# Kernel optimization log

Hardware: AMD Instinct MI355X
Metric: run time of the kernel (lower is better)

## Reference

```python
import jax, jax.numpy as jnp
import numpy as np

NUM_CLASSES = 2
LOG2_NC = float(np.log2(NUM_CLASSES))


def _conv(x, w, b=None):
    # NCHW conv, stride 1, SAME padding (kernel 3 pad 1 or kernel 1 pad 0)
    y = jax.lax.conv_general_dilated(x, w, (1, 1), 'SAME',
                                     dimension_numbers=('NCHW', 'OIHW', 'NCHW'))
    if b is not None:
        y = y + b[None, :, None, None]
    return y


def _uncertainty_map(ds):
    # entropy over class dim, thresholded to {0,1}
    logp = jax.nn.log_softmax(ds, axis=1)            # [B,C,H,W]
    prob = jnp.exp(logp)
    # torch uses log2(prob + 1e-6); replicate exactly
    ent = -jnp.sum(prob * jnp.log2(prob + 1e-6), axis=1) / LOG2_NC  # [B,H,W]
    return (ent >= 0.001).astype(jnp.float32)


def _unob(tar, amap):
    # vectorized UnoB with S=3: interior pixels with tar!=0 get pro=0 unless
    # 4*tar == sum of the 4-neighborhood (i.e. locally constant label)
    t = tar  # [B,H,W] int
    nb = t[:, 2:, 1:-1] + t[:, :-2, 1:-1] + t[:, 1:-1, 2:] + t[:, 1:-1, :-2]
    center = t[:, 1:-1, 1:-1]
    inner_pro = jnp.where((center != 0) & (4 * center != nb), 0.0, 1.0)
    pro = jnp.ones_like(amap)
    pro = pro.at[:, 1:-1, 1:-1].set(inner_pro)
    return amap * pro


def setup_inputs() -> dict:
    key = jax.random.key(0)
    ks = jax.random.split(key, 6)
    B, C, H, W = 8, 128, 128, 128
    return {
        'x': jax.random.normal(ks[0], (B, C, H, W), jnp.float32),
        'skip': jax.random.normal(ks[1], (B, C, H, W), jnp.float32),
        'tar': jax.random.randint(ks[2], (B, 1, H, W), 0, NUM_CLASSES, jnp.int64)
            if jax.config.jax_enable_x64 else
            jax.random.randint(ks[2], (B, 1, H, W), 0, NUM_CLASSES).astype(jnp.int32),
        'W1': jax.random.normal(ks[3], (128, 256, 3, 3), jnp.float32) * 0.05,
        'b1': jnp.zeros((128,), jnp.float32),
        'W2': jax.random.normal(ks[4], (128, 128, 3, 3), jnp.float32) * 0.05,
        'b2': jnp.zeros((128,), jnp.float32),
        'Wds': jax.random.normal(ks[5], (NUM_CLASSES, 128, 1, 1), jnp.float32) * 0.05,
    }


def reference(x, skip, tar, W1, b1, W2, b2, Wds):
    h = jnp.concatenate([x, skip], axis=1)            # [B,2*dim,H,W]
    h = jax.nn.leaky_relu(_conv(h, W1, b1), 0.01)     # [B,dim,H,W]
    h = jax.nn.leaky_relu(_conv(h, W2, b2), 0.01)
    ds = _conv(h, Wds)                                # [B,num_classes,H,W]
    amap = _uncertainty_map(ds)                       # [B,H,W]
    amap = _unob(tar[:, 0], amap)                     # UnoB refinement, S=3
    return h, ds, amap
```

## Files before the change

kernel.cpp:

```cpp
#include <hip/hip_runtime.h>

typedef float f32x16 __attribute__((ext_vector_type(16)));
typedef short bf16x8 __attribute__((ext_vector_type(8)));
typedef unsigned int u32;

static __device__ __forceinline__ unsigned short f2bf(float f) {
  union { float f; unsigned int u; } v;
  v.f = f;
  return (unsigned short)((v.u + 0x7FFFu + ((v.u >> 16) & 1u)) >> 16);
}

static __device__ __forceinline__ void gl_lds16(const unsigned short* g,
                                                unsigned short* l) {
  __builtin_amdgcn_global_load_lds(
      (const __attribute__((address_space(1))) u32*)g,
      (__attribute__((address_space(3))) u32*)l, 16, 0, 0);
}

#define VMCNT4 asm volatile("s_waitcnt vmcnt(4)" ::: "memory")
#define VMCNT0 asm volatile("s_waitcnt vmcnt(0)" ::: "memory")
#define LGKM0 asm volatile("s_waitcnt lgkmcnt(0)" ::: "memory")
#define BAR __builtin_amdgcn_s_barrier()
#define SCHEDB __builtin_amdgcn_sched_barrier(0)

__global__ __launch_bounds__(256) void convert_weights(
    const float* __restrict__ W1, const float* __restrict__ W2,
    unsigned short* __restrict__ W1b, unsigned short* __restrict__ W2b,
    unsigned short* __restrict__ zp) {
  if (blockIdx.x == 1728) {
    uint4* z = (uint4*)zp;
    z[threadIdx.x] = make_uint4(0, 0, 0, 0);
    z[256 + threadIdx.x] = make_uint4(0, 0, 0, 0);
    return;
  }
  int i = blockIdx.x * 256 + threadIdx.x;
  if (i < 294912) {
    int e = i & 7, co = (i >> 3) & 127, r = i >> 10;
    int tap = r % 9, pc = r / 9;
    int ci = (pc >> 1) * 16 + (pc & 1) * 8 + e;
    W1b[i] = f2bf(W1[(co * 256 + ci) * 9 + tap]);
  } else {
    int j = i - 294912;
    if (j < 147456) {
      int e = j & 7, co = (j >> 3) & 127, r = j >> 10;
      int tap = r % 9, pc = r / 9;
      int ci = (pc >> 1) * 16 + (pc & 1) * 8 + e;
      W2b[j] = f2bf(W2[(co * 128 + ci) * 9 + tap]);
    }
  }
}

__global__ __launch_bounds__(256) void transpose_to_bf16(
    const float* __restrict__ src, unsigned short* __restrict__ dst, int cigb) {
  int row = blockIdx.x;
  int b = row >> 7, y = row & 127;
  const float* s = src + (long)b * 128 * 16384 + (long)y * 128;
  for (int it = 0; it < 8; ++it) {
    int u = it * 256 + (int)threadIdx.x;
    int cig = u >> 7, px = u & 127;
    unsigned short pk[8];
#pragma unroll
    for (int e = 0; e < 8; ++e)
      pk[e] = f2bf(s[(long)(cig * 8 + e) * 16384 + px]);
    uint4 vv;
    vv.x = (unsigned)pk[0] | ((unsigned)pk[1] << 16);
    vv.y = (unsigned)pk[2] | ((unsigned)pk[3] << 16);
    vv.z = (unsigned)pk[4] | ((unsigned)pk[5] << 16);
    vv.w = (unsigned)pk[6] | ((unsigned)pk[7] << 16);
    *(uint4*)(&dst[(((long)row * 32 + cigb + cig) * 130 + px + 1) * 8]) = vv;
  }
  if (cigb == 0 && threadIdx.x < 64) {
    int g = threadIdx.x >> 1;
    long col = (threadIdx.x & 1) * 129L;
    *(uint4*)(&dst[(((long)row * 32 + g) * 130 + col) * 8]) = make_uint4(0, 0, 0, 0);
  }
}

template <int CIN, bool FUSE_DS>
__global__ __launch_bounds__(256, 2) void conv3x3(
    const unsigned short* __restrict__ src,
    const unsigned short* __restrict__ wt,
    const float* __restrict__ bias,
    const unsigned short* __restrict__ zp,
    unsigned short* __restrict__ dst_bf16,
    float* __restrict__ dst_f32,
    const float* __restrict__ wds,
    const int* __restrict__ tar,
    float* __restrict__ ds,
    float* __restrict__ amap) {
  constexpr int CPG = CIN / 8;
  constexpr int NC = CIN / 16;
  __shared__ unsigned short in_tile[2][1040 * 8];
  __shared__ unsigned short wt_tile[2304 * 8];
  __shared__ float sb[128];
  __shared__ float w0s[128], w1s[128];
  __shared__ float sc[2 * 4 * 2 * 32];

  const int tid = threadIdx.x;
  const int b = blockIdx.x >> 6;
  const int y0 = (blockIdx.x & 63) * 2;
  const int lane = tid & 63, wave = tid >> 6;
  const int wco = wave & 1, wrow = wave >> 1;
  const int l31 = lane & 31, kh = lane >> 5;

  if (tid < 128) {
    sb[tid] = bias[tid];
    if constexpr (FUSE_DS) {
      w0s[tid] = wds[tid];
      w1s[tid] = wds[128 + tid];
    }
  }

#define STAGE_IN(cic, bufi)                                                    \
  {                                                                            \
    _Pragma("unroll") for (int j = 0; j < 4; ++j) {                            \
      int o = wave * 4 + j;                                                    \
      int s = o * 64 + lane;                                                   \
      int p = s >= 520;                                                        \
      int r = s - p * 520;                                                     \
      int hy = r / 130;                                                        \
      int hx = r - hy * 130;                                                   \
      int gy = y0 - 1 + hy;                                                    \
      const unsigned short* g =                                                \
          (gy >= 0 && gy < 128)                                                \
              ? src + ((size_t)((b * 128 + gy) * CPG) + (size_t)(cic)*2 + p) * \
                          1040 +                                               \
                    hx * 8                                                     \
              : zp + lane * 8;                                                 \
      gl_lds16(g, &in_tile[bufi][(size_t)o * 512]);                            \
    }                                                                          \
  }

#define STAGE_WT(cic)                                                          \
  {                                                                            \
    const unsigned short* wslab = wt + (size_t)(cic)*18432;                    \
    _Pragma("unroll") for (int j = 0; j < 9; ++j) {                            \
      int o = wave * 9 + j;                                                    \
      gl_lds16(wslab + o * 512 + lane * 8, &wt_tile[(size_t)o * 512]);         \
    }                                                                          \
  }

#define LOAD_TAIL(cic, v)                                                      \
  {                                                                            \
    if (tid < 16) {                                                            \
      int gy_ = y0 + 2;                                                        \
      if (gy_ < 128)                                                           \
        v = *(const uint4*)(src +                                              \
                            ((size_t)((b * 128 + gy_) * CPG) +                 \
                             (size_t)(cic)*2 + 1) *                            \
                                1040 +                                         \
                            (114 + tid) * 8);                                  \
    }                                                                          \
  }

#define WRITE_TAIL(bufi, v)                                                    \
  {                                                                            \
    if (tid < 16) *(uint4*)(&in_tile[bufi][(size_t)(1024 + tid) * 8]) = v;     \
  }

  f32x16 acc[2][4] = {};

  {
    uint4 tv = make_uint4(0, 0, 0, 0);
    LOAD_TAIL(0, tv);
    STAGE_IN(0, 0);
    VMCNT0;
    WRITE_TAIL(0, tv);
    LGKM0;
    BAR;
    SCHEDB;
  }

  for (int cic = 0; cic < NC; ++cic) {
    const int cur = cic & 1;
    const bool more = (cic + 1 < NC);
    uint4 tl = make_uint4(0, 0, 0, 0);
    if (more) LOAD_TAIL(cic + 1, tl);
    STAGE_WT(cic);
    if (more) {
      STAGE_IN(cic + 1, cur ^ 1);
      VMCNT4;
      SCHEDB;
      WRITE_TAIL(cur ^ 1, tl);
    } else {
      VMCNT0;
      SCHEDB;
    }
    LGKM0;
    BAR;
    SCHEDB;

    const unsigned short* it = in_tile[cur];
    const size_t wb = (size_t)kh * 9216;
    const size_t ib = (size_t)kh * 4160;
#pragma unroll
    for (int ky = 0; ky < 3; ++ky) {
      const int hy = ky + wrow;
#pragma unroll
      for (int kx = 0; kx < 3; ++kx) {
        const int t = ky * 3 + kx;
        bf16x8 a0 = *(const bf16x8*)(&wt_tile[wb + (size_t)(t * 128 + wco * 64 + l31) * 8]);
        bf16x8 a1 = *(const bf16x8*)(&wt_tile[wb + (size_t)(t * 128 + wco * 64 + 32 + l31) * 8]);
        bf16x8 b0 = *(const bf16x8*)(&it[ib + (size_t)(hy * 130 + l31 + kx) * 8]);
        bf16x8 b1 = *(const bf16x8*)(&it[ib + (size_t)(hy * 130 + 32 + l31 + kx) * 8]);
        bf16x8 b2 = *(const bf16x8*)(&it[ib + (size_t)(hy * 130 + 64 + l31 + kx) * 8]);
        bf16x8 b3 = *(const bf16x8*)(&it[ib + (size_t)(hy * 130 + 96 + l31 + kx) * 8]);
        acc[0][0] = __builtin_amdgcn_mfma_f32_32x32x16_bf16(a0, b0, acc[0][0], 0, 0, 0);
        acc[0][1] = __builtin_amdgcn_mfma_f32_32x32x16_bf16(a0, b1, acc[0][1], 0, 0, 0);
        acc[0][2] = __builtin_amdgcn_mfma_f32_32x32x16_bf16(a0, b2, acc[0][2], 0, 0, 0);
        acc[0][3] = __builtin_amdgcn_mfma_f32_32x32x16_bf16(a0, b3, acc[0][3], 0, 0, 0);
        acc[1][0] = __builtin_amdgcn_mfma_f32_32x32x16_bf16(a1, b0, acc[1][0], 0, 0, 0);
        acc[1][1] = __builtin_amdgcn_mfma_f32_32x32x16_bf16(a1, b1, acc[1][1], 0, 0, 0);
        acc[1][2] = __builtin_amdgcn_mfma_f32_32x32x16_bf16(a1, b2, acc[1][2], 0, 0, 0);
        acc[1][3] = __builtin_amdgcn_mfma_f32_32x32x16_bf16(a1, b3, acc[1][3], 0, 0, 0);
      }
    }
    SCHEDB;
    LGKM0;
    BAR;
    SCHEDB;
  }

  const int gyo = y0 + wrow;
  float pd[4][2] = {};
#pragma unroll
  for (int fc = 0; fc < 2; ++fc) {
#pragma unroll
    for (int fp = 0; fp < 4; ++fp) {
      const int px = fp * 32 + l31;
      if constexpr (!FUSE_DS) {
#pragma unroll
        for (int rg = 0; rg < 4; ++rg) {
          const int co0 = wco * 64 + fc * 32 + rg * 8 + kh * 4;
          unsigned short pk[4];
#pragma unroll
          for (int q = 0; q < 4; ++q) {
            float v = acc[fc][fp][rg * 4 + q] + sb[co0 + q];
            v = v > 0.f ? v : 0.01f * v;
            pk[q] = f2bf(v);
          }
          uint2 o;
          o.x = (unsigned)pk[0] | ((unsigned)pk[1] << 16);
          o.y = (unsigned)pk[2] | ((unsigned)pk[3] << 16);
          *(uint2*)(&dst_bf16[(((long)(b * 128 + gyo) * 16 + (co0 >> 3)) * 130 + px + 1) * 8 +
                              kh * 4]) = o;
        }
      } else {
#pragma unroll
        for (int rg = 0; rg < 4; ++rg) {
          const int co0 = wco * 64 + fc * 32 + rg * 8 + kh * 4;
          float4 wv0 = *(const float4*)(&w0s[co0]);
          float4 wv1 = *(const float4*)(&w1s[co0]);
#pragma unroll
          for (int q = 0; q < 4; ++q) {
            float v = acc[fc][fp][rg * 4 + q] + sb[co0 + q];
            v = v > 0.f ? v : 0.01f * v;
            dst_f32[((long)(b * 128 + co0 + q) << 14) + (gyo << 7) + px] = v;
            float wq0 = (q == 0) ? wv0.x : (q == 1) ? wv0.y : (q == 2) ? wv0.z : wv0.w;
            float wq1 = (q == 0) ? wv1.x : (q == 1) ? wv1.y : (q == 2) ? wv1.z : wv1.w;
            pd[fp][0] += wq0 * v;
            pd[fp][1] += wq1 * v;
          }
        }
      }
    }
  }

  if constexpr (!FUSE_DS) {
    if (tid < 64) {
      int row = tid >> 5, g = (tid >> 1) & 15;
      long col = (tid & 1) * 129L;
      *(uint4*)(&dst_bf16[(((long)(b * 128 + y0 + row) * 16 + g) * 130 + col) * 8]) =
          make_uint4(0, 0, 0, 0);
    }
  } else {
#pragma unroll
    for (int fp = 0; fp < 4; ++fp)
#pragma unroll
      for (int c = 0; c < 2; ++c)
        pd[fp][c] += __shfl_xor(pd[fp][c], 32, 64);
    if (wco == 1 && kh == 0) {
#pragma unroll
      for (int fp = 0; fp < 4; ++fp)
#pragma unroll
        for (int c = 0; c < 2; ++c)
          sc[((wrow * 4 + fp) * 2 + c) * 32 + l31] = pd[fp][c];
    }
    __syncthreads();
    if (wco == 0 && kh == 0) {
      const int* tb = tar + (long)b * 16384;
#pragma unroll
      for (int fp = 0; fp < 4; ++fp) {
        const int px = fp * 32 + l31;
        float a0 = pd[fp][0] + sc[((wrow * 4 + fp) * 2 + 0) * 32 + l31];
        float a1 = pd[fp][1] + sc[((wrow * 4 + fp) * 2 + 1) * 32 + l31];
        ds[((long)b * 2) * 16384 + (gyo << 7) + px] = a0;
        ds[((long)b * 2 + 1) * 16384 + (gyo << 7) + px] = a1;
        float m = fmaxf(a0, a1);
        float e0 = expf(a0 - m), e1 = expf(a1 - m);
        float s = e0 + e1;
        float p0f = e0 / s, p1f = e1 / s;
        float ent = -(p0f * log2f(p0f + 1e-6f) + p1f * log2f(p1f + 1e-6f));
        float un = ent >= 0.001f ? 1.f : 0.f;
        float pro = 1.f;
        if (gyo > 0 && gyo < 127 && px > 0 && px < 127) {
          int c = tb[(gyo << 7) + px];
          if (c != 0) {
            int nb2 = tb[((gyo - 1) << 7) + px] + tb[((gyo + 1) << 7) + px] +
                      tb[(gyo << 7) + px - 1] + tb[(gyo << 7) + px + 1];
            if (4 * c != nb2) pro = 0.f;
          }
        }
        amap[((long)(b * 128 + gyo) << 7) + px] = un * pro;
      }
    }
  }
#undef STAGE_IN
#undef STAGE_WT
#undef LOAD_TAIL
#undef WRITE_TAIL
}

extern "C" void kernel_launch(void* const* d_in, const int* in_sizes, int n_in,
                              void* d_out, int out_size, void* d_ws, size_t ws_size,
                              hipStream_t stream) {
  const float* x    = (const float*)d_in[0];
  const float* skip = (const float*)d_in[1];
  const int*   tar  = (const int*)d_in[2];
  const float* W1   = (const float*)d_in[3];
  const float* b1   = (const float*)d_in[4];
  const float* W2   = (const float*)d_in[5];
  const float* b2   = (const float*)d_in[6];
  const float* Wds  = (const float*)d_in[7];

  float* out_h  = (float*)d_out;
  float* out_ds = out_h + 16777216;
  float* out_am = out_ds + 262144;

  unsigned short* W1b = (unsigned short*)d_ws;
  unsigned short* W2b = W1b + 294912;
  unsigned short* zp  = W2b + 147456;
  unsigned short* h1  = (unsigned short*)((char*)d_ws + (1u << 20));

  unsigned short* h0 = (unsigned short*)d_out;

  convert_weights<<<1729, 256, 0, stream>>>(W1, W2, W1b, W2b, zp);
  transpose_to_bf16<<<1024, 256, 0, stream>>>(x, h0, 0);
  transpose_to_bf16<<<1024, 256, 0, stream>>>(skip, h0, 16);
  conv3x3<256, false><<<512, 256, 0, stream>>>(h0, W1b, b1, zp, h1, nullptr,
                                               nullptr, nullptr, nullptr, nullptr);
  conv3x3<128, true><<<512, 256, 0, stream>>>(h1, W2b, b2, zp, nullptr, out_h,
                                              Wds, tar, out_ds, out_am);
}
```

Before: 154.9 us.

## Double conv tile to 4 rows with 512 threads and double-buffer weight staging

Each conv block now covers 4 output rows with 8 waves instead of 2 rows with 4 waves, so each staged weight slab is reused across twice as many output pixels and the grid drops to 256 blocks. Weights are now double-buffered alongside the input tile, and all async global-to-LDS copies are precomputed into per-thread base pointers and strides, issued 8 per thread each iteration. The separate tail-load path for the halo is removed. The cost is more LDS per block, which can limit occupancy, and only 256 blocks to spread over the GPU's compute units.

```diff
diff --git a/kernel.cpp b/kernel.cpp
--- a/kernel.cpp
+++ b/kernel.cpp
@@ -17,7 +17,7 @@
       (__attribute__((address_space(3))) u32*)l, 16, 0, 0);
 }
 
-#define VMCNT4 asm volatile("s_waitcnt vmcnt(4)" ::: "memory")
+#define VMCNT8 asm volatile("s_waitcnt vmcnt(8)" ::: "memory")
 #define VMCNT0 asm volatile("s_waitcnt vmcnt(0)" ::: "memory")
 #define LGKM0 asm volatile("s_waitcnt lgkmcnt(0)" ::: "memory")
 #define BAR __builtin_amdgcn_s_barrier()
@@ -77,7 +77,7 @@
 }
 
 template <int CIN, bool FUSE_DS>
-__global__ __launch_bounds__(256, 2) void conv3x3(
+__global__ __launch_bounds__(512, 2) void conv3x3(
     const unsigned short* __restrict__ src,
     const unsigned short* __restrict__ wt,
     const float* __restrict__ bias,
@@ -90,15 +90,16 @@
     float* __restrict__ amap) {
   constexpr int CPG = CIN / 8;
   constexpr int NC = CIN / 16;
-  __shared__ unsigned short in_tile[2][1040 * 8];
-  __shared__ unsigned short wt_tile[2304 * 8];
+  __shared__ unsigned short in_tile[2][1664 * 8];
+  __shared__ unsigned short wt_tile[2][2304 * 8];
+  __shared__ unsigned short scr[64 * 8];
   __shared__ float sb[128];
   __shared__ float w0s[128], w1s[128];
-  __shared__ float sc[2 * 4 * 2 * 32];
+  __shared__ float sc[4 * 4 * 2 * 32];
 
   const int tid = threadIdx.x;
-  const int b = blockIdx.x >> 6;
-  const int y0 = (blockIdx.x & 63) * 2;
+  const int b = blockIdx.x >> 5;
+  const int y0 = (blockIdx.x & 31) * 4;
   const int lane = tid & 63, wave = tid >> 6;
   const int wco = wave & 1, wrow = wave >> 1;
   const int l31 = lane & 31, kh = lane >> 5;
@@ -111,96 +112,77 @@
     }
   }
 
-#define STAGE_IN(cic, bufi)                                                    \
-  {                                                                            \
-    _Pragma("unroll") for (int j = 0; j < 4; ++j) {                            \
-      int o = wave * 4 + j;                                                    \
-      int s = o * 64 + lane;                                                   \
-      int p = s >= 520;                                                        \
-      int r = s - p * 520;                                                     \
-      int hy = r / 130;                                                        \
-      int hx = r - hy * 130;                                                   \
-      int gy = y0 - 1 + hy;                                                    \
-      const unsigned short* g =                                                \
-          (gy >= 0 && gy < 128)                                                \
-              ? src + ((size_t)((b * 128 + gy) * CPG) + (size_t)(cic)*2 + p) * \
-                          1040 +                                               \
-                    hx * 8                                                     \
-              : zp + lane * 8;                                                 \
-      gl_lds16(g, &in_tile[bufi][(size_t)o * 512]);                            \
-    }                                                                          \
-  }
-
-#define STAGE_WT(cic)                                                          \
-  {                                                                            \
-    const unsigned short* wslab = wt + (size_t)(cic)*18432;                    \
-    _Pragma("unroll") for (int j = 0; j < 9; ++j) {                            \
-      int o = wave * 9 + j;                                                    \
-      gl_lds16(wslab + o * 512 + lane * 8, &wt_tile[(size_t)o * 512]);         \
-    }                                                                          \
-  }
-
-#define LOAD_TAIL(cic, v)                                                      \
-  {                                                                            \
-    if (tid < 16) {                                                            \
-      int gy_ = y0 + 2;                                                        \
-      if (gy_ < 128)                                                           \
-        v = *(const uint4*)(src +                                              \
-                            ((size_t)((b * 128 + gy_) * CPG) +                 \
-                             (size_t)(cic)*2 + 1) *                            \
-                                1040 +                                         \
-                            (114 + tid) * 8);                                  \
-    }                                                                          \
-  }
-
-#define WRITE_TAIL(bufi, v)                                                    \
-  {                                                                            \
-    if (tid < 16) *(uint4*)(&in_tile[bufi][(size_t)(1024 + tid) * 8]) = v;     \
+  const unsigned short* gb[8];
+  unsigned short* ld0[8];
+  int gst[8];
+  int lst[8];
+#pragma unroll
+  for (int i = 0; i < 8; ++i) {
+    const int o = wave * 8 + i;
+    if (o < 36) {
+      gb[i] = wt + o * 512 + lane * 8;
+      gst[i] = 18432;
+      ld0[i] = &wt_tile[0][(size_t)o * 512];
+      lst[i] = 18432;
+    } else if (o < 62) {
+      const int q = o - 36;
+      const int p = q / 13, j = q - p * 13;
+      const int s = j * 64 + lane;
+      const int hy = s / 130, hx = s - hy * 130;
+      const int gy = y0 - 1 + hy;
+      const bool ok = (s < 780) && (gy >= 0) && (gy < 128);
+      gb[i] = ok ? src + ((size_t)((b * 128 + gy) * CPG) + p) * 1040 + hx * 8
+                 : zp + lane * 8;
+      gst[i] = ok ? 2080 : 0;
+      ld0[i] = &in_tile[0][(size_t)(p * 832 + j * 64) * 8];
+      lst[i] = 1664 * 8;
+    } else {
+      gb[i] = zp + lane * 8;
+      gst[i] = 0;
+      ld0[i] = &scr[0];
+      lst[i] = 0;
+    }
   }
 
   f32x16 acc[2][4] = {};
 
-  {
-    uint4 tv = make_uint4(0, 0, 0, 0);
-    LOAD_TAIL(0, tv);
-    STAGE_IN(0, 0);
-    VMCNT0;
-    WRITE_TAIL(0, tv);
-    LGKM0;
-    BAR;
-    SCHEDB;
-  }
+#pragma unroll
+  for (int i = 0; i < 8; ++i) gl_lds16(gb[i], ld0[i]);
+  VMCNT0;
+  LGKM0;
+  BAR;
+  SCHEDB;
 
   for (int cic = 0; cic < NC; ++cic) {
     const int cur = cic & 1;
     const bool more = (cic + 1 < NC);
-    uint4 tl = make_uint4(0, 0, 0, 0);
-    if (more) LOAD_TAIL(cic + 1, tl);
-    STAGE_WT(cic);
     if (more) {
-      STAGE_IN(cic + 1, cur ^ 1);
-      VMCNT4;
+      const int nb = cur ^ 1;
+#pragma unroll
+      for (int i = 0; i < 8; ++i)
+        gl_lds16(gb[i] + (size_t)(cic + 1) * gst[i],
+                 ld0[i] + (size_t)nb * lst[i]);
       SCHEDB;
-      WRITE_TAIL(cur ^ 1, tl);
+      VMCNT8;
     } else {
       VMCNT0;
-      SCHEDB;
-    }
-    LGKM0;
+    }
+    SCHEDB;
     BAR;
     SCHEDB;
 
-    const unsigned short* it = in_tile[cur];
+    const unsigned short* it = &in_tile[cur][0];
+    const unsigned short* wl = &wt_tile[cur][0];
+    const size_t ib = (size_t)kh * (832 * 8);
     const size_t wb = (size_t)kh * 9216;
-    const size_t ib = (size_t)kh * 4160;
 #pragma unroll
     for (int ky = 0; ky < 3; ++ky) {
       const int hy = ky + wrow;
 #pragma unroll
       for (int kx = 0; kx < 3; ++kx) {
         const int t = ky * 3 + kx;
-        bf16x8 a0 = *(const bf16x8*)(&wt_tile[wb + (size_t)(t * 128 + wco * 64 + l31) * 8]);
-        bf16x8 a1 = *(const bf16x8*)(&wt_tile[wb + (size_t)(t * 128 + wco * 64 + 32 + l31) * 8]);
+        bf16x8 a0 = *(const bf16x8*)(&wl[wb + (size_t)(t * 128 + wco * 64 + l31) * 8]);
+        bf16x8 a1 = *(const bf16x8*)(&wl[wb + (size_t)(t * 128 + wco * 64 + 32 + l31) * 8]);
         bf16x8 b0 = *(const bf16x8*)(&it[ib + (size_t)(hy * 130 + l31 + kx) * 8]);
         bf16x8 b1 = *(const bf16x8*)(&it[ib + (size_t)(hy * 130 + 32 + l31 + kx) * 8]);
         bf16x8 b2 = *(const bf16x8*)(&it[ib + (size_t)(hy * 130 + 64 + l31 + kx) * 8]);
@@ -267,7 +249,7 @@
   }
 
   if constexpr (!FUSE_DS) {
-    if (tid < 64) {
+    if (tid < 128) {
       int row = tid >> 5, g = (tid >> 1) & 15;
       long col = (tid & 1) * 129L;
       *(uint4*)(&dst_bf16[(((long)(b * 128 + y0 + row) * 16 + g) * 130 + col) * 8]) =
@@ -315,10 +297,6 @@
       }
     }
   }
-#undef STAGE_IN
-#undef STAGE_WT
-#undef LOAD_TAIL
-#undef WRITE_TAIL
 }
 
 extern "C" void kernel_launch(void* const* d_in, const int* in_sizes, int n_in,
@@ -347,8 +325,8 @@
   convert_weights<<<1729, 256, 0, stream>>>(W1, W2, W1b, W2b, zp);
   transpose_to_bf16<<<1024, 256, 0, stream>>>(x, h0, 0);
   transpose_to_bf16<<<1024, 256, 0, stream>>>(skip, h0, 16);
-  conv3x3<256, false><<<512, 256, 0, stream>>>(h0, W1b, b1, zp, h1, nullptr,
+  conv3x3<256, false><<<256, 512, 0, stream>>>(h0, W1b, b1, zp, h1, nullptr,
                                                nullptr, nullptr, nullptr, nullptr);
-  conv3x3<128, true><<<512, 256, 0, stream>>>(h1, W2b, b2, zp, nullptr, out_h,
+  conv3x3<128, true><<<256, 512, 0, stream>>>(h1, W2b, b2, zp, nullptr, out_h,
                                               Wds, tar, out_ds, out_am);
 }
```

After: 150.4 us. 2.9% less time.

## Load conv weights directly to registers with prefetch, remap blocks, merge transposes

Applied to the files above, without the earlier changes.

Removes the LDS weight tile from the 3x3 conv kernels. Each lane now loads its weight fragments straight from global memory into registers, prefetching the next kernel row (and the next channel chunk's first row) during the current MFMAs. This cuts LDS traffic and VMEM-to-LDS staging and shrinks shared memory use. It also swizzles the block index so consecutive blocks fall on different batches, and merges the two transpose launches into one. The risks are higher register pressure and global-load latency that now sits on the critical path.

```diff
diff --git a/kernel.cpp b/kernel.cpp
--- a/kernel.cpp
+++ b/kernel.cpp
@@ -51,8 +51,12 @@
 }
 
 __global__ __launch_bounds__(256) void transpose_to_bf16(
-    const float* __restrict__ src, unsigned short* __restrict__ dst, int cigb) {
-  int row = blockIdx.x;
+    const float* __restrict__ x, const float* __restrict__ skip,
+    unsigned short* __restrict__ dst) {
+  int bid = blockIdx.x;
+  const float* src = (bid < 1024) ? x : skip;
+  int cigb = (bid < 1024) ? 0 : 16;
+  int row = bid & 1023;
   int b = row >> 7, y = row & 127;
   const float* s = src + (long)b * 128 * 16384 + (long)y * 128;
   for (int it = 0; it < 8; ++it) {
@@ -91,14 +95,14 @@
   constexpr int CPG = CIN / 8;
   constexpr int NC = CIN / 16;
   __shared__ unsigned short in_tile[2][1040 * 8];
-  __shared__ unsigned short wt_tile[2304 * 8];
   __shared__ float sb[128];
   __shared__ float w0s[128], w1s[128];
   __shared__ float sc[2 * 4 * 2 * 32];
 
   const int tid = threadIdx.x;
-  const int b = blockIdx.x >> 6;
-  const int y0 = (blockIdx.x & 63) * 2;
+  const int wg = (blockIdx.x & 7) * 64 + (blockIdx.x >> 3);
+  const int b = wg >> 6;
+  const int y0 = (wg & 63) * 2;
   const int lane = tid & 63, wave = tid >> 6;
   const int wco = wave & 1, wrow = wave >> 1;
   const int l31 = lane & 31, kh = lane >> 5;
@@ -131,15 +135,6 @@
     }                                                                          \
   }
 
-#define STAGE_WT(cic)                                                          \
-  {                                                                            \
-    const unsigned short* wslab = wt + (size_t)(cic)*18432;                    \
-    _Pragma("unroll") for (int j = 0; j < 9; ++j) {                            \
-      int o = wave * 9 + j;                                                    \
-      gl_lds16(wslab + o * 512 + lane * 8, &wt_tile[(size_t)o * 512]);         \
-    }                                                                          \
-  }
-
 #define LOAD_TAIL(cic, v)                                                      \
   {                                                                            \
     if (tid < 16) {                                                            \
@@ -160,6 +155,9 @@
 
   f32x16 acc[2][4] = {};
 
+  const unsigned short* wlane =
+      wt + (size_t)kh * 9216 + (size_t)(wco * 64 + l31) * 8;
+
   {
     uint4 tv = make_uint4(0, 0, 0, 0);
     LOAD_TAIL(0, tv);
@@ -170,50 +168,70 @@
     BAR;
     SCHEDB;
   }
+  bf16x8 a0[3], a1[3];
+#pragma unroll
+  for (int t = 0; t < 3; ++t) {
+    a0[t] = *(const bf16x8*)(wlane + t * 1024);
+    a1[t] = *(const bf16x8*)(wlane + t * 1024 + 256);
+  }
 
   for (int cic = 0; cic < NC; ++cic) {
-    const int cur = cic & 1;
+    const int cur = cic & 1, nbuf = cur ^ 1;
     const bool more = (cic + 1 < NC);
     uint4 tl = make_uint4(0, 0, 0, 0);
-    if (more) LOAD_TAIL(cic + 1, tl);
-    STAGE_WT(cic);
+    SCHEDB;
     if (more) {
-      STAGE_IN(cic + 1, cur ^ 1);
+      LOAD_TAIL(cic + 1, tl);
+      STAGE_IN(cic + 1, nbuf);
+      SCHEDB;
       VMCNT4;
       SCHEDB;
-      WRITE_TAIL(cur ^ 1, tl);
+      WRITE_TAIL(nbuf, tl);
     } else {
       VMCNT0;
-      SCHEDB;
     }
     LGKM0;
     BAR;
     SCHEDB;
 
-    const unsigned short* it = in_tile[cur];
-    const size_t wb = (size_t)kh * 9216;
+    const unsigned short* wl = wlane + (size_t)cic * 18432;
+    const unsigned short* wlnext = wlane + (size_t)(more ? cic + 1 : cic) * 18432;
+    const unsigned short* it = &in_tile[cur][0];
     const size_t ib = (size_t)kh * 4160;
 #pragma unroll
     for (int ky = 0; ky < 3; ++ky) {
       const int hy = ky + wrow;
+      bf16x8 n0[3], n1[3];
+      if (ky < 2) {
+#pragma unroll
+        for (int t = 0; t < 3; ++t) {
+          n0[t] = *(const bf16x8*)(wl + (ky * 3 + 3 + t) * 1024);
+          n1[t] = *(const bf16x8*)(wl + (ky * 3 + 3 + t) * 1024 + 256);
+        }
+      } else {
+#pragma unroll
+        for (int t = 0; t < 3; ++t) {
+          n0[t] = *(const bf16x8*)(wlnext + t * 1024);
+          n1[t] = *(const bf16x8*)(wlnext + t * 1024 + 256);
+        }
+      }
 #pragma unroll
       for (int kx = 0; kx < 3; ++kx) {
-        const int t = ky * 3 + kx;
-        bf16x8 a0 = *(const bf16x8*)(&wt_tile[wb + (size_t)(t * 128 + wco * 64 + l31) * 8]);
-        bf16x8 a1 = *(const bf16x8*)(&wt_tile[wb + (size_t)(t * 128 + wco * 64 + 32 + l31) * 8]);
         bf16x8 b0 = *(const bf16x8*)(&it[ib + (size_t)(hy * 130 + l31 + kx) * 8]);
         bf16x8 b1 = *(const bf16x8*)(&it[ib + (size_t)(hy * 130 + 32 + l31 + kx) * 8]);
         bf16x8 b2 = *(const bf16x8*)(&it[ib + (size_t)(hy * 130 + 64 + l31 + kx) * 8]);
         bf16x8 b3 = *(const bf16x8*)(&it[ib + (size_t)(hy * 130 + 96 + l31 + kx) * 8]);
-        acc[0][0] = __builtin_amdgcn_mfma_f32_32x32x16_bf16(a0, b0, acc[0][0], 0, 0, 0);
-        acc[0][1] = __builtin_amdgcn_mfma_f32_32x32x16_bf16(a0, b1, acc[0][1], 0, 0, 0);
-        acc[0][2] = __builtin_amdgcn_mfma_f32_32x32x16_bf16(a0, b2, acc[0][2], 0, 0, 0);
-        acc[0][3] = __builtin_amdgcn_mfma_f32_32x32x16_bf16(a0, b3, acc[0][3], 0, 0, 0);
-        acc[1][0] = __builtin_amdgcn_mfma_f32_32x32x16_bf16(a1, b0, acc[1][0], 0, 0, 0);
-        acc[1][1] = __builtin_amdgcn_mfma_f32_32x32x16_bf16(a1, b1, acc[1][1], 0, 0, 0);
-        acc[1][2] = __builtin_amdgcn_mfma_f32_32x32x16_bf16(a1, b2, acc[1][2], 0, 0, 0);
-        acc[1][3] = __builtin_amdgcn_mfma_f32_32x32x16_bf16(a1, b3, acc[1][3], 0, 0, 0);
+        acc[0][0] = __builtin_amdgcn_mfma_f32_32x32x16_bf16(a0[kx], b0, acc[0][0], 0, 0, 0);
+        acc[0][1] = __builtin_amdgcn_mfma_f32_32x32x16_bf16(a0[kx], b1, acc[0][1], 0, 0, 0);
+        acc[0][2] = __builtin_amdgcn_mfma_f32_32x32x16_bf16(a0[kx], b2, acc[0][2], 0, 0, 0);
+        acc[0][3] = __builtin_amdgcn_mfma_f32_32x32x16_bf16(a0[kx], b3, acc[0][3], 0, 0, 0);
+        acc[1][0] = __builtin_amdgcn_mfma_f32_32x32x16_bf16(a1[kx], b0, acc[1][0], 0, 0, 0);
+        acc[1][1] = __builtin_amdgcn_mfma_f32_32x32x16_bf16(a1[kx], b1, acc[1][1], 0, 0, 0);
+        acc[1][2] = __builtin_amdgcn_mfma_f32_32x32x16_bf16(a1[kx], b2, acc[1][2], 0, 0, 0);
+        acc[1][3] = __builtin_amdgcn_mfma_f32_32x32x16_bf16(a1[kx], b3, acc[1][3], 0, 0, 0);
       }
+#pragma unroll
+      for (int t = 0; t < 3; ++t) { a0[t] = n0[t]; a1[t] = n1[t]; }
     }
     SCHEDB;
     LGKM0;
@@ -292,12 +310,12 @@
 #pragma unroll
       for (int fp = 0; fp < 4; ++fp) {
         const int px = fp * 32 + l31;
-        float a0 = pd[fp][0] + sc[((wrow * 4 + fp) * 2 + 0) * 32 + l31];
-        float a1 = pd[fp][1] + sc[((wrow * 4 + fp) * 2 + 1) * 32 + l31];
-        ds[((long)b * 2) * 16384 + (gyo << 7) + px] = a0;
-        ds[((long)b * 2 + 1) * 16384 + (gyo << 7) + px] = a1;
-        float m = fmaxf(a0, a1);
-        float e0 = expf(a0 - m), e1 = expf(a1 - m);
+        float a0f = pd[fp][0] + sc[((wrow * 4 + fp) * 2 + 0) * 32 + l31];
+        float a1f = pd[fp][1] + sc[((wrow * 4 + fp) * 2 + 1) * 32 + l31];
+        ds[((long)b * 2) * 16384 + (gyo << 7) + px] = a0f;
+        ds[((long)b * 2 + 1) * 16384 + (gyo << 7) + px] = a1f;
+        float m = fmaxf(a0f, a1f);
+        float e0 = expf(a0f - m), e1 = expf(a1f - m);
         float s = e0 + e1;
         float p0f = e0 / s, p1f = e1 / s;
         float ent = -(p0f * log2f(p0f + 1e-6f) + p1f * log2f(p1f + 1e-6f));
@@ -316,7 +334,6 @@
     }
   }
 #undef STAGE_IN
-#undef STAGE_WT
 #undef LOAD_TAIL
 #undef WRITE_TAIL
 }
@@ -345,8 +362,7 @@
   unsigned short* h0 = (unsigned short*)d_out;
 
   convert_weights<<<1729, 256, 0, stream>>>(W1, W2, W1b, W2b, zp);
-  transpose_to_bf16<<<1024, 256, 0, stream>>>(x, h0, 0);
-  transpose_to_bf16<<<1024, 256, 0, stream>>>(skip, h0, 16);
+  transpose_to_bf16<<<2048, 256, 0, stream>>>(x, skip, h0);
   conv3x3<256, false><<<512, 256, 0, stream>>>(h0, W1b, b1, zp, h1, nullptr,
                                                nullptr, nullptr, nullptr, nullptr);
   conv3x3<128, true><<<512, 256, 0, stream>>>(h1, W2b, b2, zp, nullptr, out_h,
```

Result: faster. 151.1 us (-2.4%).
